# Optimization experiments

Measured on AMD Instinct MI355X. Metric: run time of the kernel, lower is better.

Reference implementation:

```python
import jax, jax.numpy as jnp
import numpy as np
from jax import lax

DT = 0.01
INPUT_SCALER = 20.0
BETA1 = 1.0


def setup_inputs() -> dict:
    key = jax.random.key(0)
    k1, k2, k3 = jax.random.split(key, 3)
    bs, T, d, nk = 8, 64, 32, 32
    X_r = jax.random.normal(k1, (bs, T, d, d, nk), dtype=jnp.float32)
    X_i = jax.random.normal(k2, (bs, T, d, d, nk), dtype=jnp.float32)
    # omegas ~ U(min_omega, max_omega) * 2*pi (Gaussian blur omitted: it only
    # smooths the fixed parameter initialization, not the forward math)
    min_omega, max_omega = 0.1, 1.0
    omegas = (jax.random.uniform(k3, (d, d, nk), dtype=jnp.float32)
              * (max_omega - min_omega) + min_omega) * (2 * 3.1415)
    return {"X_r": X_r, "X_i": X_i, "omegas": omegas}


def reference(X_r, X_i, omegas):
    bs, T, d1, d2, nk = X_r.shape
    # time-major for scan: [T, bs, d, d, nk]
    Xr_t = jnp.moveaxis(X_r, 1, 0)
    Xi_t = jnp.moveaxis(X_i, 1, 0)

    r0 = jnp.ones((bs, d1, d2, nk), dtype=X_r.dtype)
    phi0 = jnp.zeros((bs, d1, d2, nk), dtype=X_r.dtype)

    def step(carry, xs):
        r, phi = carry
        xr, xi = xs
        input_r = INPUT_SCALER * xr * jnp.cos(phi)
        input_phi = INPUT_SCALER * xi * jnp.sin(phi)
        r = r + ((1.0 - BETA1 * r * r) * r + input_r) * DT
        phi = phi + (omegas - input_phi) * DT
        return (r, phi), (r, phi)

    _, (r_arr, phi_arr) = lax.scan(step, (r0, phi0), (Xr_t, Xi_t))
    # back to batch-major: [bs, T, d, d, nk]
    r_arr = jnp.moveaxis(r_arr, 0, 1)
    phi_arr = jnp.moveaxis(phi_arr, 0, 1)
    return r_arr * jnp.cos(phi_arr), r_arr * jnp.sin(phi_arr)
```

## Files before the change

kernel.cpp:

```cpp
#include <hip/hip_runtime.h>


#define T_STEPS 64
#define CH      32768
#define BS      8

__global__ __launch_bounds__(256)
void hopf_scan_kernel(const float2* __restrict__ Xr,
                      const float2* __restrict__ Xi,
                      const float2* __restrict__ Om,
                      float2* __restrict__ out)
{
    const float DT = 0.01f;
    const float SC = 20.0f;

    int tid = blockIdx.x * blockDim.x + threadIdx.x;
    int b   = tid >> 14;
    int cp  = tid & 16383;

    float2 omega = Om[cp];

    const size_t stride = CH / 2;
    size_t base = (size_t)(b * T_STEPS) * stride + cp;
    const float2* pxr = Xr + base;
    const float2* pxi = Xi + base;
    float2* po0 = out + base;
    float2* po1 = po0 + (size_t)BS * T_STEPS * stride;

    float r0 = 1.f, r1 = 1.f;
    float ph0 = 0.f, ph1 = 0.f;
    float c0 = 1.f, s0 = 0.f, c1 = 1.f, s1 = 0.f;

    #pragma unroll 4
    for (int t = 0; t < T_STEPS; ++t) {
        float2 xr = pxr[(size_t)t * stride];
        float2 xi = pxi[(size_t)t * stride];

        float ir = SC * xr.x * c0;
        float ip = SC * xi.x * s0;
        r0  = r0  + ((1.f - r0 * r0) * r0 + ir) * DT;
        ph0 = ph0 + (omega.x - ip) * DT;
        sincosf(ph0, &s0, &c0);

        float jr = SC * xr.y * c1;
        float jp = SC * xi.y * s1;
        r1  = r1  + ((1.f - r1 * r1) * r1 + jr) * DT;
        ph1 = ph1 + (omega.y - jp) * DT;
        sincosf(ph1, &s1, &c1);

        po0[(size_t)t * stride] = make_float2(r0 * c0, r1 * c1);
        po1[(size_t)t * stride] = make_float2(r0 * s0, r1 * s1);
    }
}

extern "C" void kernel_launch(void* const* d_in, const int* in_sizes, int n_in,
                              void* d_out, int out_size, void* d_ws, size_t ws_size,
                              hipStream_t stream) {
    const float2* Xr = (const float2*)d_in[0];
    const float2* Xi = (const float2*)d_in[1];
    const float2* Om = (const float2*)d_in[2];
    float2* out = (float2*)d_out;

    dim3 block(256);
    dim3 grid((BS * CH / 2) / 256);
    hopf_scan_kernel<<<grid, block, 0, stream>>>(Xr, Xi, Om, out);
}
```

Before: 250.4 us.

## Use one channel per thread with register prefetch and nontemporal stores

Each thread now handles one scalar channel instead of a float2 pair, which doubles the thread count. Inputs for the next four timesteps are loaded into registers ahead of the compute on the current group, and outputs are written with nontemporal stores. The aim is more memory parallelism and latency hiding on a bandwidth-bound scan, at the cost of narrower 4-byte accesses and more registers for the prefetch buffers.

```diff
diff --git a/kernel.cpp b/kernel.cpp
--- a/kernel.cpp
+++ b/kernel.cpp
@@ -4,64 +4,75 @@
 #define T_STEPS 64
 #define CH      32768
 #define BS      8
+#define PF      4
 
 __global__ __launch_bounds__(256)
-void hopf_scan_kernel(const float2* __restrict__ Xr,
-                      const float2* __restrict__ Xi,
-                      const float2* __restrict__ Om,
-                      float2* __restrict__ out)
+void hopf_scan_kernel(const float* __restrict__ Xr,
+                      const float* __restrict__ Xi,
+                      const float* __restrict__ Om,
+                      float* __restrict__ out)
 {
     const float DT = 0.01f;
     const float SC = 20.0f;
 
     int tid = blockIdx.x * blockDim.x + threadIdx.x;
-    int b   = tid >> 14;
-    int cp  = tid & 16383;
+    int b   = tid >> 15;
+    int c   = tid & (CH - 1);
 
-    float2 omega = Om[cp];
+    float omega = Om[c];
 
-    const size_t stride = CH / 2;
-    size_t base = (size_t)(b * T_STEPS) * stride + cp;
-    const float2* pxr = Xr + base;
-    const float2* pxi = Xi + base;
-    float2* po0 = out + base;
-    float2* po1 = po0 + (size_t)BS * T_STEPS * stride;
+    const size_t stride = CH;
+    size_t base = (size_t)(b * T_STEPS) * stride + c;
+    const float* pxr = Xr + base;
+    const float* pxi = Xi + base;
+    float* po0 = out + base;
+    float* po1 = po0 + (size_t)BS * T_STEPS * stride;
 
-    float r0 = 1.f, r1 = 1.f;
-    float ph0 = 0.f, ph1 = 0.f;
-    float c0 = 1.f, s0 = 0.f, c1 = 1.f, s1 = 0.f;
+    float r = 1.f, ph = 0.f, co = 1.f, si = 0.f;
 
-    #pragma unroll 4
-    for (int t = 0; t < T_STEPS; ++t) {
-        float2 xr = pxr[(size_t)t * stride];
-        float2 xi = pxi[(size_t)t * stride];
+    float xr[PF], xi[PF];
+    #pragma unroll
+    for (int i = 0; i < PF; ++i) {
+        xr[i] = pxr[(size_t)i * stride];
+        xi[i] = pxi[(size_t)i * stride];
+    }
 
-        float ir = SC * xr.x * c0;
-        float ip = SC * xi.x * s0;
-        r0  = r0  + ((1.f - r0 * r0) * r0 + ir) * DT;
-        ph0 = ph0 + (omega.x - ip) * DT;
-        sincosf(ph0, &s0, &c0);
+    for (int t0 = 0; t0 < T_STEPS; t0 += PF) {
+        float nxr[PF], nxi[PF];
+        if (t0 + PF < T_STEPS) {
+            #pragma unroll
+            for (int i = 0; i < PF; ++i) {
+                nxr[i] = pxr[(size_t)(t0 + PF + i) * stride];
+                nxi[i] = pxi[(size_t)(t0 + PF + i) * stride];
+            }
+        }
 
-        float jr = SC * xr.y * c1;
-        float jp = SC * xi.y * s1;
-        r1  = r1  + ((1.f - r1 * r1) * r1 + jr) * DT;
-        ph1 = ph1 + (omega.y - jp) * DT;
-        sincosf(ph1, &s1, &c1);
+        #pragma unroll
+        for (int i = 0; i < PF; ++i) {
+            float ir = SC * xr[i] * co;
+            float ip = SC * xi[i] * si;
+            r  = r  + ((1.f - r * r) * r + ir) * DT;
+            ph = ph + (omega - ip) * DT;
+            sincosf(ph, &si, &co);
+            size_t off = (size_t)(t0 + i) * stride;
+            __builtin_nontemporal_store(r * co, po0 + off);
+            __builtin_nontemporal_store(r * si, po1 + off);
+        }
 
-        po0[(size_t)t * stride] = make_float2(r0 * c0, r1 * c1);
-        po1[(size_t)t * stride] = make_float2(r0 * s0, r1 * s1);
+        #pragma unroll
+        for (int i = 0; i < PF; ++i) { xr[i] = nxr[i]; xi[i] = nxi[i]; }
     }
 }
 
 extern "C" void kernel_launch(void* const* d_in, const int* in_sizes, int n_in,
                               void* d_out, int out_size, void* d_ws, size_t ws_size,
                               hipStream_t stream) {
-    const float2* Xr = (const float2*)d_in[0];
-    const float2* Xi = (const float2*)d_in[1];
-    const float2* Om = (const float2*)d_in[2];
-    float2* out = (float2*)d_out;
+    const float* Xr = (const float*)d_in[0];
+    const float* Xi = (const float*)d_in[1];
+    const float* Om = (const float*)d_in[2];
+    float* out = (float*)d_out;
 
     dim3 block(256);
-    dim3 grid((BS * CH / 2) / 256);
+    dim3 grid(BS * CH / 256);
     hopf_scan_kernel<<<grid, block, 0, stream>>>(Xr, Xi, Om, out);
 }
```

Result: faster. 239.1 us (-4.5%).
